# Optimization experiments

Measured on AMD Instinct MI355X. Metric: run time of the kernel, lower is better.

## Reference

```python
import jax, jax.numpy as jnp
import numpy as np

D_MODEL = 1024
NUM_HEADS = 16
D_K = D_MODEL // NUM_HEADS
SCALE = float(np.sqrt(D_K))


def setup_inputs() -> dict:
    key = jax.random.key(0)
    ks = jax.random.split(key, 11)
    B, S, D = 4, 2048, D_MODEL
    w_std = 1.0 / np.sqrt(D)
    inp = {
        "query": jax.random.normal(ks[0], (B, S, D), jnp.float32),
        "key": jax.random.normal(ks[1], (B, S, D), jnp.float32),
        "value": jax.random.normal(ks[2], (B, S, D), jnp.float32),
        "wq": jax.random.normal(ks[3], (D, D), jnp.float32) * w_std,
        "bq": jax.random.normal(ks[4], (D,), jnp.float32) * w_std,
        "wk": jax.random.normal(ks[5], (D, D), jnp.float32) * w_std,
        "bk": jax.random.normal(ks[6], (D,), jnp.float32) * w_std,
        "wv": jax.random.normal(ks[7], (D, D), jnp.float32) * w_std,
        "bv": jax.random.normal(ks[8], (D,), jnp.float32) * w_std,
        "wo": jax.random.normal(ks[9], (D, D), jnp.float32) * w_std,
        "bo": jax.random.normal(ks[10], (D,), jnp.float32) * w_std,
    }
    return inp


def reference(query, key, value, wq, bq, wk, bk, wv, bv, wo, bo):
    B, Sq, D = query.shape
    H, dk = NUM_HEADS, D_K
    # linear projections (weights stored as [in, out])
    q = query @ wq + bq
    k = key @ wk + bk
    v = value @ wv + bv
    # [B, H, S, d_k]
    q = q.reshape(B, Sq, H, dk).transpose(0, 2, 1, 3)
    k = k.reshape(B, -1, H, dk).transpose(0, 2, 1, 3)
    v = v.reshape(B, -1, H, dk).transpose(0, 2, 1, 3)
    # full attention scores [B, H, Sq, Sk]
    att = jnp.einsum("bhqd,bhkd->bhqk", q, k) / SCALE
    att = jax.nn.softmax(att, axis=-1)
    out = jnp.einsum("bhqk,bhkd->bhqd", att, v)
    out = out.transpose(0, 2, 1, 3).reshape(B, Sq, D)
    return out @ wo + bo
```

## Files before the change

kernel.cpp:

```cpp
#include <hip/hip_runtime.h>


typedef _Float16 fp16;
typedef fp16  fp16x8 __attribute__((ext_vector_type(8)));
typedef fp16  fp16x4 __attribute__((ext_vector_type(4)));
typedef float f32x4  __attribute__((ext_vector_type(4)));

#define NROWS 8192
#define DM    1024
#define SEQ   2048
#define DK    64
#define LOG2E 1.44269504088896340736f

__device__ __forceinline__ f32x4 mfma16x16(fp16x8 a, fp16x8 b, f32x4 c) {
    return __builtin_amdgcn_mfma_f32_16x16x32_f16(a, b, c, 0, 0, 0);
}

__device__ __forceinline__ void gload16(const fp16* g, fp16* l) {
    __builtin_amdgcn_global_load_lds(
        (const __attribute__((address_space(1))) void*)g,
        (__attribute__((address_space(3))) void*)l, 16, 0, 0);
}

__global__ __launch_bounds__(256) void cast_fp16_kernel(
    const float* __restrict__ x, fp16* __restrict__ y, int n4) {
    int i = blockIdx.x * 256 + threadIdx.x;
    if (i >= n4) return;
    const float4 v = ((const float4*)x)[i];
    fp16x4 o;
    o[0] = (fp16)v.x; o[1] = (fp16)v.y; o[2] = (fp16)v.z; o[3] = (fp16)v.w;
    ((fp16x4*)y)[i] = o;
}

__global__ __launch_bounds__(256) void transpose_w_kernel(
    const float* __restrict__ W, fp16* __restrict__ T) {
    __shared__ float tile[32][33];
    const int tx = threadIdx.x, ty = threadIdx.y;
    const int bx = blockIdx.x * 32, by = blockIdx.y * 32;
#pragma unroll
    for (int j = 0; j < 4; ++j)
        tile[ty + 8 * j][tx] = W[(size_t)(by + ty + 8 * j) * DM + bx + tx];
    __syncthreads();
#pragma unroll
    for (int j = 0; j < 4; ++j)
        T[(size_t)(bx + ty + 8 * j) * DM + by + tx] = (fp16)tile[tx][ty + 8 * j];
}

template<int OUTMODE>
__global__ __launch_bounds__(256) void gemm_kernel(
    const fp16* __restrict__ A, const fp16* __restrict__ B,
    const float* __restrict__ bias, float oscale, void* __restrict__ outp) {
    const int tid = threadIdx.x;
    const int lane = tid & 63;
    const int w = tid >> 6;
    const int wr = w >> 1, wc = w & 1;
    const int li = lane & 15, lg = lane >> 4;
    const int m0 = blockIdx.y * 128, n0 = blockIdx.x * 128;
    const int lrow = lane >> 3;
    const int lch  = (lane & 7) ^ lrow;

    __shared__ fp16 At[128 * 64];
    __shared__ fp16 Bt[128 * 64];

    f32x4 acc[4][4] = {};

    for (int k0 = 0; k0 < DM; k0 += 64) {
        __syncthreads();
#pragma unroll
        for (int it = 0; it < 4; ++it) {
            int R = (w * 4 + it) * 8 + lrow;
            gload16(&A[(size_t)(m0 + R) * DM + k0 + lch * 8], &At[(w * 4 + it) * 512]);
            gload16(&B[(size_t)(n0 + R) * DM + k0 + lch * 8], &Bt[(w * 4 + it) * 512]);
        }
        __syncthreads();
        fp16x8 af[4][2], bfr[4][2];
#pragma unroll
        for (int mf = 0; mf < 4; ++mf)
#pragma unroll
            for (int ks = 0; ks < 2; ++ks)
                af[mf][ks] = *(const fp16x8*)&At[(wr * 64 + mf * 16 + li) * 64 +
                                                 (((ks * 4 + lg) ^ (li & 7)) * 8)];
#pragma unroll
        for (int nf = 0; nf < 4; ++nf)
#pragma unroll
            for (int ks = 0; ks < 2; ++ks)
                bfr[nf][ks] = *(const fp16x8*)&Bt[(wc * 64 + nf * 16 + li) * 64 +
                                                  (((ks * 4 + lg) ^ (li & 7)) * 8)];
#pragma unroll
        for (int ks = 0; ks < 2; ++ks)
#pragma unroll
            for (int mf = 0; mf < 4; ++mf)
#pragma unroll
                for (int nf = 0; nf < 4; ++nf)
                    acc[mf][nf] = mfma16x16(af[mf][ks], bfr[nf][ks], acc[mf][nf]);
    }
#pragma unroll
    for (int nf = 0; nf < 4; ++nf) {
        int col = n0 + wc * 64 + nf * 16 + li;
        float bv = bias[col];
        if (OUTMODE == 2) {
#pragma unroll
            for (int mf = 0; mf < 4; ++mf) {
                int rowb = m0 + wr * 64 + mf * 16 + lg * 4;
                fp16x4 pk;
#pragma unroll
                for (int r = 0; r < 4; ++r)
                    pk[r] = (fp16)((acc[mf][nf][r] + bv) * oscale);
                size_t o = ((size_t)(rowb >> 11) * 1024 + col) * SEQ + (rowb & 2047);
                *(fp16x4*)&((fp16*)outp)[o] = pk;
            }
        } else {
#pragma unroll
            for (int mf = 0; mf < 4; ++mf) {
#pragma unroll
                for (int r = 0; r < 4; ++r) {
                    int row = m0 + wr * 64 + mf * 16 + lg * 4 + r;
                    float v = (acc[mf][nf][r] + bv) * oscale;
                    if (OUTMODE == 1) ((float*)outp)[(size_t)row * DM + col] = v;
                    else              ((fp16*)outp)[(size_t)row * DM + col] = (fp16)v;
                }
            }
        }
    }
}

__global__ __launch_bounds__(512) void attn_kernel(
    const fp16* __restrict__ Qb, const fp16* __restrict__ Kb,
    const fp16* __restrict__ Vtg, fp16* __restrict__ Of) {
    const int tid = threadIdx.x;
    const int lane = tid & 63;
    const int w = tid >> 6;
    const int li = lane & 15, lg = lane >> 4;

    int L = blockIdx.x;
    L = (L & 7) * 64 + (L >> 3);
    const int qt = L & 7, bh = L >> 3;
    const int b = bh >> 4, h = bh & 15;
    const size_t rowQ = (size_t)b * SEQ + (size_t)qt * 256;
    const int c0 = h * DK;

    __shared__ fp16 Kt[64 * 64];
    __shared__ fp16 Vt[64 * 64];
    __shared__ fp16 Pl[8][32 * 64];

    fp16x8 qf[2][2];
#pragma unroll
    for (int mf = 0; mf < 2; ++mf)
#pragma unroll
        for (int ks = 0; ks < 2; ++ks)
            qf[mf][ks] = *(const fp16x8*)&Qb[(rowQ + w * 32 + mf * 16 + li) * DM +
                                             c0 + ks * 32 + lg * 8];

    fp16x8 ones;
#pragma unroll
    for (int j = 0; j < 8; ++j) ones[j] = (fp16)1.0f;

    f32x4 oacc[2][4] = {};
    f32x4 lacc[2] = {};

    const int sr = tid >> 3, sc = tid & 7;
    const int ssl = sc ^ (sr & 7);
    fp16x8 rk, rv;
    rk = *(const fp16x8*)&Kb[((size_t)b * SEQ + sr) * DM + c0 + sc * 8];
    rv = *(const fp16x8*)&Vtg[((size_t)bh * 64 + sr) * SEQ + sc * 8];

    for (int kt = 0; kt < SEQ / 64; ++kt) {
        *(fp16x8*)&Kt[sr * 64 + ssl * 8] = rk;
        *(fp16x8*)&Vt[sr * 64 + ssl * 8] = rv;
        __syncthreads();
        if (kt + 1 < SEQ / 64) {
            rk = *(const fp16x8*)&Kb[((size_t)b * SEQ + (kt + 1) * 64 + sr) * DM + c0 + sc * 8];
            rv = *(const fp16x8*)&Vtg[((size_t)bh * 64 + sr) * SEQ + (kt + 1) * 64 + sc * 8];
        }

        f32x4 s[4][2] = {};
        __builtin_amdgcn_s_setprio(1);
#pragma unroll
        for (int nf = 0; nf < 4; ++nf)
#pragma unroll
            for (int ks = 0; ks < 2; ++ks) {
                fp16x8 kf = *(const fp16x8*)&Kt[(nf * 16 + li) * 64 +
                                                (((ks * 4 + lg) ^ (li & 7)) * 8)];
#pragma unroll
                for (int mf = 0; mf < 2; ++mf)
                    s[nf][mf] = mfma16x16(kf, qf[mf][ks], s[nf][mf]);
            }
        __builtin_amdgcn_s_setprio(0);

#pragma unroll
        for (int mf = 0; mf < 2; ++mf) {
            fp16x4 pk[4];
#pragma unroll
            for (int nf = 0; nf < 4; ++nf)
#pragma unroll
                for (int r = 0; r < 4; ++r)
                    pk[nf][r] = (fp16)__builtin_amdgcn_exp2f(s[nf][mf][r]);
            int row = mf * 16 + li;
#pragma unroll
            for (int nf = 0; nf < 4; ++nf) {
                int sl = (nf * 2 + (lg >> 1)) ^ (li & 7);
                *(fp16x4*)&Pl[w][row * 64 + sl * 8 + (lg & 1) * 4] = pk[nf];
            }
        }

        __builtin_amdgcn_s_setprio(1);
#pragma unroll
        for (int ks = 0; ks < 2; ++ks) {
            fp16x8 pf[2];
#pragma unroll
            for (int mf = 0; mf < 2; ++mf) {
                pf[mf] = *(const fp16x8*)&Pl[w][(mf * 16 + li) * 64 +
                                                (((ks * 4 + lg) ^ (li & 7)) * 8)];
                lacc[mf] = mfma16x16(pf[mf], ones, lacc[mf]);
            }
#pragma unroll
            for (int nf = 0; nf < 4; ++nf) {
                fp16x8 vf = *(const fp16x8*)&Vt[(nf * 16 + li) * 64 +
                                                (((ks * 4 + lg) ^ (li & 7)) * 8)];
#pragma unroll
                for (int mf = 0; mf < 2; ++mf)
                    oacc[mf][nf] = mfma16x16(pf[mf], vf, oacc[mf][nf]);
            }
        }
        __builtin_amdgcn_s_setprio(0);
        __syncthreads();
    }

#pragma unroll
    for (int mf = 0; mf < 2; ++mf) {
#pragma unroll
        for (int r = 0; r < 4; ++r) {
            float linv = 1.0f / lacc[mf][r];
            size_t row = rowQ + w * 32 + mf * 16 + lg * 4 + r;
#pragma unroll
            for (int nf = 0; nf < 4; ++nf) {
                int col = c0 + nf * 16 + li;
                Of[row * DM + col] = (fp16)(oacc[mf][nf][r] * linv);
            }
        }
    }
}

extern "C" void kernel_launch(void* const* d_in, const int* in_sizes, int n_in,
                              void* d_out, int out_size, void* d_ws, size_t ws_size,
                              hipStream_t stream) {
    const float* query = (const float*)d_in[0];
    const float* key   = (const float*)d_in[1];
    const float* value = (const float*)d_in[2];
    const float* wq    = (const float*)d_in[3];
    const float* bq    = (const float*)d_in[4];
    const float* wk    = (const float*)d_in[5];
    const float* bk    = (const float*)d_in[6];
    const float* wv    = (const float*)d_in[7];
    const float* bv    = (const float*)d_in[8];
    const float* wo    = (const float*)d_in[9];
    const float* bo    = (const float*)d_in[10];

    char* ws = (char*)d_ws;
    const size_t SZX = (size_t)NROWS * DM * 2;
    const size_t SZW = (size_t)DM * DM * 2;
    fp16* Xb  = (fp16*)(ws);
    fp16* Wt  = (fp16*)(ws + SZX);
    fp16* Qb  = (fp16*)(ws + SZX + SZW);
    fp16* Kb  = (fp16*)(ws + 2 * SZX + SZW);
    fp16* Vtg = (fp16*)(ws + 3 * SZX + SZW);
    fp16* Of  = Xb;

    const dim3 bT(32, 8), gT(32, 32);
    const dim3 gemmG(8, 64);
    const int n4 = NROWS * DM / 4;

    cast_fp16_kernel<<<8192, 256, 0, stream>>>(query, Xb, n4);
    transpose_w_kernel<<<gT, bT, 0, stream>>>(wq, Wt);
    gemm_kernel<0><<<gemmG, 256, 0, stream>>>(Xb, Wt, bq, 0.125f * LOG2E, Qb);
    cast_fp16_kernel<<<8192, 256, 0, stream>>>(key, Xb, n4);
    transpose_w_kernel<<<gT, bT, 0, stream>>>(wk, Wt);
    gemm_kernel<0><<<gemmG, 256, 0, stream>>>(Xb, Wt, bk, 1.0f, Kb);
    cast_fp16_kernel<<<8192, 256, 0, stream>>>(value, Xb, n4);
    transpose_w_kernel<<<gT, bT, 0, stream>>>(wv, Wt);
    gemm_kernel<2><<<gemmG, 256, 0, stream>>>(Xb, Wt, bv, 1.0f, Vtg);
    attn_kernel<<<512, 512, 0, stream>>>(Qb, Kb, Vtg, Of);
    transpose_w_kernel<<<gT, bT, 0, stream>>>(wo, Wt);
    gemm_kernel<1><<<gemmG, 256, 0, stream>>>(Of, Wt, bo, 1.0f, (float*)d_out);
}
```

Before: 235.1 us.

## Batch QKV casts/GEMMs into single launches, double-buffer attention K/V, narrower output GEMM tile

```diff
diff --git a/kernel.cpp b/kernel.cpp
--- a/kernel.cpp
+++ b/kernel.cpp
@@ -11,6 +11,7 @@
 #define SEQ   2048
 #define DK    64
 #define LOG2E 1.44269504088896340736f
+#define QSCALE (0.125f * LOG2E)
 
 __device__ __forceinline__ f32x4 mfma16x16(fp16x8 a, fp16x8 b, f32x4 c) {
     return __builtin_amdgcn_mfma_f32_16x16x32_f16(a, b, c, 0, 0, 0);
@@ -23,7 +24,13 @@
 }
 
 __global__ __launch_bounds__(256) void cast_fp16_kernel(
-    const float* __restrict__ x, fp16* __restrict__ y, int n4) {
+    const float* __restrict__ x0, const float* __restrict__ x1,
+    const float* __restrict__ x2,
+    fp16* __restrict__ y0, fp16* __restrict__ y1, fp16* __restrict__ y2,
+    int n4) {
+    const int z = blockIdx.y;
+    const float* x = (z == 0) ? x0 : (z == 1) ? x1 : x2;
+    fp16*       y = (z == 0) ? y0 : (z == 1) ? y1 : y2;
     int i = blockIdx.x * 256 + threadIdx.x;
     if (i >= n4) return;
     const float4 v = ((const float4*)x)[i];
@@ -33,7 +40,13 @@
 }
 
 __global__ __launch_bounds__(256) void transpose_w_kernel(
-    const float* __restrict__ W, fp16* __restrict__ T) {
+    const float* __restrict__ w0, const float* __restrict__ w1,
+    const float* __restrict__ w2, const float* __restrict__ w3,
+    fp16* __restrict__ t0, fp16* __restrict__ t1,
+    fp16* __restrict__ t2, fp16* __restrict__ t3) {
+    const int z = blockIdx.z;
+    const float* W = (z == 0) ? w0 : (z == 1) ? w1 : (z == 2) ? w2 : w3;
+    fp16*       T = (z == 0) ? t0 : (z == 1) ? t1 : (z == 2) ? t2 : t3;
     __shared__ float tile[32][33];
     const int tx = threadIdx.x, ty = threadIdx.y;
     const int bx = blockIdx.x * 32, by = blockIdx.y * 32;
@@ -46,10 +59,22 @@
         T[(size_t)(bx + ty + 8 * j) * DM + by + tx] = (fp16)tile[tx][ty + 8 * j];
 }
 
-template<int OUTMODE>
-__global__ __launch_bounds__(256) void gemm_kernel(
-    const fp16* __restrict__ A, const fp16* __restrict__ B,
-    const float* __restrict__ bias, float oscale, void* __restrict__ outp) {
+__global__ __launch_bounds__(256) void gemm_qkv_kernel(
+    const fp16* __restrict__ Xq, const fp16* __restrict__ Xk,
+    const fp16* __restrict__ Xv,
+    const fp16* __restrict__ Wq, const fp16* __restrict__ Wk,
+    const fp16* __restrict__ Wv,
+    const float* __restrict__ bq, const float* __restrict__ bk,
+    const float* __restrict__ bv,
+    fp16* __restrict__ Qb, fp16* __restrict__ Kb, fp16* __restrict__ Vtg,
+    int zbase) {
+    const int z = blockIdx.z + zbase;
+    const fp16* __restrict__ A = (z == 0) ? Xq : (z == 1) ? Xk : Xv;
+    const fp16* __restrict__ B = (z == 0) ? Wq : (z == 1) ? Wk : Wv;
+    const float* __restrict__ bias = (z == 0) ? bq : (z == 1) ? bk : bv;
+    fp16* __restrict__ outp = (z == 0) ? Qb : (z == 1) ? Kb : Vtg;
+    const float oscale = (z == 0) ? QSCALE : 1.0f;
+
     const int tid = threadIdx.x;
     const int lane = tid & 63;
     const int w = tid >> 6;
@@ -97,30 +122,91 @@
 #pragma unroll
     for (int nf = 0; nf < 4; ++nf) {
         int col = n0 + wc * 64 + nf * 16 + li;
-        float bv = bias[col];
-        if (OUTMODE == 2) {
+        float bv_ = bias[col];
+        if (z == 2) {
 #pragma unroll
             for (int mf = 0; mf < 4; ++mf) {
                 int rowb = m0 + wr * 64 + mf * 16 + lg * 4;
                 fp16x4 pk;
 #pragma unroll
                 for (int r = 0; r < 4; ++r)
-                    pk[r] = (fp16)((acc[mf][nf][r] + bv) * oscale);
+                    pk[r] = (fp16)(acc[mf][nf][r] + bv_);
                 size_t o = ((size_t)(rowb >> 11) * 1024 + col) * SEQ + (rowb & 2047);
-                *(fp16x4*)&((fp16*)outp)[o] = pk;
+                *(fp16x4*)&outp[o] = pk;
             }
         } else {
 #pragma unroll
-            for (int mf = 0; mf < 4; ++mf) {
+            for (int mf = 0; mf < 4; ++mf)
 #pragma unroll
                 for (int r = 0; r < 4; ++r) {
                     int row = m0 + wr * 64 + mf * 16 + lg * 4 + r;
-                    float v = (acc[mf][nf][r] + bv) * oscale;
-                    if (OUTMODE == 1) ((float*)outp)[(size_t)row * DM + col] = v;
-                    else              ((fp16*)outp)[(size_t)row * DM + col] = (fp16)v;
+                    outp[(size_t)row * DM + col] = (fp16)((acc[mf][nf][r] + bv_) * oscale);
                 }
-            }
-        }
+        }
+    }
+}
+
+__global__ __launch_bounds__(256) void gemm_out_kernel(
+    const fp16* __restrict__ A, const fp16* __restrict__ B,
+    const float* __restrict__ bias, float* __restrict__ outp) {
+    const int tid = threadIdx.x;
+    const int lane = tid & 63;
+    const int w = tid >> 6;
+    const int wr = w >> 1, wc = w & 1;
+    const int li = lane & 15, lg = lane >> 4;
+    const int m0 = blockIdx.y * 128, n0 = blockIdx.x * 64;
+    const int lrow = lane >> 3;
+    const int lch  = (lane & 7) ^ lrow;
+
+    __shared__ fp16 At[128 * 64];
+    __shared__ fp16 Bt[64 * 64];
+
+    f32x4 acc[4][2] = {};
+
+    for (int k0 = 0; k0 < DM; k0 += 64) {
+        __syncthreads();
+#pragma unroll
+        for (int it = 0; it < 4; ++it) {
+            int R = (w * 4 + it) * 8 + lrow;
+            gload16(&A[(size_t)(m0 + R) * DM + k0 + lch * 8], &At[(w * 4 + it) * 512]);
+            if (it < 2) {
+                int Rb = (w * 2 + it) * 8 + lrow;
+                gload16(&B[(size_t)(n0 + Rb) * DM + k0 + lch * 8], &Bt[(w * 2 + it) * 512]);
+            }
+        }
+        __syncthreads();
+        fp16x8 af[4][2], bfr[2][2];
+#pragma unroll
+        for (int mf = 0; mf < 4; ++mf)
+#pragma unroll
+            for (int ks = 0; ks < 2; ++ks)
+                af[mf][ks] = *(const fp16x8*)&At[(wr * 64 + mf * 16 + li) * 64 +
+                                                 (((ks * 4 + lg) ^ (li & 7)) * 8)];
+#pragma unroll
+        for (int nf = 0; nf < 2; ++nf)
+#pragma unroll
+            for (int ks = 0; ks < 2; ++ks)
+                bfr[nf][ks] = *(const fp16x8*)&Bt[(wc * 32 + nf * 16 + li) * 64 +
+                                                  (((ks * 4 + lg) ^ (li & 7)) * 8)];
+#pragma unroll
+        for (int ks = 0; ks < 2; ++ks)
+#pragma unroll
+            for (int mf = 0; mf < 4; ++mf)
+#pragma unroll
+                for (int nf = 0; nf < 2; ++nf)
+                    acc[mf][nf] = mfma16x16(af[mf][ks], bfr[nf][ks], acc[mf][nf]);
+    }
+#pragma unroll
+    for (int nf = 0; nf < 2; ++nf) {
+        int col = n0 + wc * 32 + nf * 16 + li;
+        float bv_ = bias[col];
+#pragma unroll
+        for (int mf = 0; mf < 4; ++mf)
+#pragma unroll
+            for (int r = 0; r < 4; ++r) {
+                int row = m0 + wr * 64 + mf * 16 + lg * 4 + r;
+                outp[(size_t)row * DM + col] = acc[mf][nf][r] + bv_;
+            }
     }
 }
 
@@ -139,8 +225,8 @@
     const size_t rowQ = (size_t)b * SEQ + (size_t)qt * 256;
     const int c0 = h * DK;
 
-    __shared__ fp16 Kt[64 * 64];
-    __shared__ fp16 Vt[64 * 64];
+    __shared__ fp16 Kt[2][64 * 64];
+    __shared__ fp16 Vt[2][64 * 64];
     __shared__ fp16 Pl[8][32 * 64];
 
     fp16x8 qf[2][2];
@@ -163,12 +249,14 @@
     fp16x8 rk, rv;
     rk = *(const fp16x8*)&Kb[((size_t)b * SEQ + sr) * DM + c0 + sc * 8];
     rv = *(const fp16x8*)&Vtg[((size_t)bh * 64 + sr) * SEQ + sc * 8];
+    *(fp16x8*)&Kt[0][sr * 64 + ssl * 8] = rk;
+    *(fp16x8*)&Vt[0][sr * 64 + ssl * 8] = rv;
+    __syncthreads();
 
     for (int kt = 0; kt < SEQ / 64; ++kt) {
-        *(fp16x8*)&Kt[sr * 64 + ssl * 8] = rk;
-        *(fp16x8*)&Vt[sr * 64 + ssl * 8] = rv;
-        __syncthreads();
-        if (kt + 1 < SEQ / 64) {
+        const int cur = kt & 1;
+        const bool more = (kt + 1 < SEQ / 64);
+        if (more) {
             rk = *(const fp16x8*)&Kb[((size_t)b * SEQ + (kt + 1) * 64 + sr) * DM + c0 + sc * 8];
             rv = *(const fp16x8*)&Vtg[((size_t)bh * 64 + sr) * SEQ + (kt + 1) * 64 + sc * 8];
         }
@@ -179,8 +267,8 @@
         for (int nf = 0; nf < 4; ++nf)
 #pragma unroll
             for (int ks = 0; ks < 2; ++ks) {
-                fp16x8 kf = *(const fp16x8*)&Kt[(nf * 16 + li) * 64 +
-                                                (((ks * 4 + lg) ^ (li & 7)) * 8)];
+                fp16x8 kf = *(const fp16x8*)&Kt[cur][(nf * 16 + li) * 64 +
+                                                     (((ks * 4 + lg) ^ (li & 7)) * 8)];
 #pragma unroll
                 for (int mf = 0; mf < 2; ++mf)
                     s[nf][mf] = mfma16x16(kf, qf[mf][ks], s[nf][mf]);
@@ -215,15 +303,20 @@
             }
 #pragma unroll
             for (int nf = 0; nf < 4; ++nf) {
-                fp16x8 vf = *(const fp16x8*)&Vt[(nf * 16 + li) * 64 +
-                                                (((ks * 4 + lg) ^ (li & 7)) * 8)];
+                fp16x8 vf = *(const fp16x8*)&Vt[cur][(nf * 16 + li) * 64 +
+                                                     (((ks * 4 + lg) ^ (li & 7)) * 8)];
 #pragma unroll
                 for (int mf = 0; mf < 2; ++mf)
                     oacc[mf][nf] = mfma16x16(pf[mf], vf, oacc[mf][nf]);
             }
         }
         __builtin_amdgcn_s_setprio(0);
-        __syncthreads();
+
+        if (more) {
+            *(fp16x8*)&Kt[cur ^ 1][sr * 64 + ssl * 8] = rk;
+            *(fp16x8*)&Vt[cur ^ 1][sr * 64 + ssl * 8] = rv;
+            __syncthreads();
+        }
     }
 
 #pragma unroll
@@ -259,27 +352,59 @@
     char* ws = (char*)d_ws;
     const size_t SZX = (size_t)NROWS * DM * 2;
     const size_t SZW = (size_t)DM * DM * 2;
-    fp16* Xb  = (fp16*)(ws);
-    fp16* Wt  = (fp16*)(ws + SZX);
-    fp16* Qb  = (fp16*)(ws + SZX + SZW);
-    fp16* Kb  = (fp16*)(ws + 2 * SZX + SZW);
-    fp16* Vtg = (fp16*)(ws + 3 * SZX + SZW);
-    fp16* Of  = Xb;
-
-    const dim3 bT(32, 8), gT(32, 32);
-    const dim3 gemmG(8, 64);
     const int n4 = NROWS * DM / 4;
-
-    cast_fp16_kernel<<<8192, 256, 0, stream>>>(query, Xb, n4);
-    transpose_w_kernel<<<gT, bT, 0, stream>>>(wq, Wt);
-    gemm_kernel<0><<<gemmG, 256, 0, stream>>>(Xb, Wt, bq, 0.125f * LOG2E, Qb);
-    cast_fp16_kernel<<<8192, 256, 0, stream>>>(key, Xb, n4);
-    transpose_w_kernel<<<gT, bT, 0, stream>>>(wk, Wt);
-    gemm_kernel<0><<<gemmG, 256, 0, stream>>>(Xb, Wt, bk, 1.0f, Kb);
-    cast_fp16_kernel<<<8192, 256, 0, stream>>>(value, Xb, n4);
-    transpose_w_kernel<<<gT, bT, 0, stream>>>(wv, Wt);
-    gemm_kernel<2><<<gemmG, 256, 0, stream>>>(Xb, Wt, bv, 1.0f, Vtg);
-    attn_kernel<<<512, 512, 0, stream>>>(Qb, Kb, Vtg, Of);
-    transpose_w_kernel<<<gT, bT, 0, stream>>>(wo, Wt);
-    gemm_kernel<1><<<gemmG, 256, 0, stream>>>(Of, Wt, bo, 1.0f, (float*)d_out);
-}
+    const dim3 bT(32, 8);
+
+    if (ws_size >= 3 * SZX + 4 * SZW + 3 * SZX) {
+        fp16* Xq  = (fp16*)(ws);
+        fp16* Xk  = (fp16*)(ws + SZX);
+        fp16* Xv  = (fp16*)(ws + 2 * SZX);
+        fp16* Wtq = (fp16*)(ws + 3 * SZX);
+        fp16* Wtk = (fp16*)(ws + 3 * SZX + SZW);
+        fp16* Wtv = (fp16*)(ws + 3 * SZX + 2 * SZW);
+        fp16* Wto = (fp16*)(ws + 3 * SZX + 3 * SZW);
+        fp16* Qb  = (fp16*)(ws + 3 * SZX + 4 * SZW);
+        fp16* Kb  = (fp16*)(ws + 4 * SZX + 4 * SZW);
+        fp16* Vtg = (fp16*)(ws + 5 * SZX + 4 * SZW);
+        fp16* Of  = Xq;
+
+        cast_fp16_kernel<<<dim3(8192, 3), 256, 0, stream>>>(
+            query, key, value, Xq, Xk, Xv, n4);
+        transpose_w_kernel<<<dim3(32, 32, 4), bT, 0, stream>>>(
+            wq, wk, wv, wo, Wtq, Wtk, Wtv, Wto);
+        gemm_qkv_kernel<<<dim3(8, 64, 3), 256, 0, stream>>>(
+            Xq, Xk, Xv, Wtq, Wtk, Wtv, bq, bk, bv, Qb, Kb, Vtg, 0);
+        attn_kernel<<<512, 512, 0, stream>>>(Qb, Kb, Vtg, Of);
+        gemm_out_kernel<<<dim3(16, 64), 256, 0, stream>>>(Of, Wto, bo, (float*)d_out);
+    } else {
+        fp16* Xb  = (fp16*)(ws);
+        fp16* Wt  = (fp16*)(ws + SZX);
+        fp16* Qb  = (fp16*)(ws + SZX + SZW);
+        fp16* Kb  = (fp16*)(ws + 2 * SZX + SZW);
+        fp16* Vtg = (fp16*)(ws + 3 * SZX + SZW);
+        fp16* Of  = Xb;
+
+        cast_fp16_kernel<<<dim3(8192, 1), 256, 0, stream>>>(
+            query, nullptr, nullptr, Xb, nullptr, nullptr, n4);
+        transpose_w_kernel<<<dim3(32, 32, 1), bT, 0, stream>>>(
+            wq, wq, wq, wq, Wt, Wt, Wt, Wt);
+        gemm_qkv_kernel<<<dim3(8, 64, 1), 256, 0, stream>>>(
+            Xb, Xb, Xb, Wt, Wt, Wt, bq, bq, bq, Qb, Qb, Qb, 0);
+        cast_fp16_kernel<<<dim3(8192, 1), 256, 0, stream>>>(
+            key, nullptr, nullptr, Xb, nullptr, nullptr, n4);
+        transpose_w_kernel<<<dim3(32, 32, 1), bT, 0, stream>>>(
+            wk, wk, wk, wk, Wt, Wt, Wt, Wt);
+        gemm_qkv_kernel<<<dim3(8, 64, 1), 256, 0, stream>>>(
+            Xb, Xb, Xb, Wt, Wt, Wt, bk, bk, bk, Kb, Kb, Kb, 1);
+        cast_fp16_kernel<<<dim3(8192, 1), 256, 0, stream>>>(
+            value, nullptr, nullptr, Xb, nullptr, nullptr, n4);
+        transpose_w_kernel<<<dim3(32, 32, 1), bT, 0, stream>>>(
+            wv, wv, wv, wv, Wt, Wt, Wt, Wt);
+        gemm_qkv_kernel<<<dim3(8, 64, 1), 256, 0, stream>>>(
+            Xb, Xb, Xb, Wt, Wt, Wt, bv, bv, bv, Vtg, Vtg, Vtg, 2);
+        attn_kernel<<<512, 512, 0, stream>>>(Qb, Kb, Vtg, Of);
+        transpose_w_kernel<<<dim3(32, 32, 1), bT, 0, stream>>>(
+            wo, wo, wo, wo, Wt, Wt, Wt, Wt);
+        gemm_out_kernel<<<dim3(16, 64), 256, 0, stream>>>(Of, Wt, bo, (float*)d_out);
+    }
+}
```

Result: faster. 227.8 us (-3.1%).
